# Performance work log

Hardware: AMD Instinct MI355X
Metric: run time of the kernel (lower is better)

The kernel has to match this reference:

```python
import jax, jax.numpy as jnp
import numpy as np

B, N, D, M, H = 16, 196, 512, 20, 8


def setup_inputs() -> dict:
    key = jax.random.key(0)
    ks = jax.random.split(key, 8)
    s = 0.02  # small init scale for stable activations
    return {
        "F_clean": jax.random.normal(ks[0], (B, N, D), dtype=jnp.float32),
        "in_proj_w": jax.random.normal(ks[1], (3 * D, D), dtype=jnp.float32) * s,
        "in_proj_b": jnp.zeros((3 * D,), jnp.float32),
        "out_w": jax.random.normal(ks[2], (D, D), dtype=jnp.float32) * s,
        "out_b": jnp.zeros((D,), jnp.float32),
        "w1": jax.random.normal(ks[3], (D, D), dtype=jnp.float32) * s,
        "b1": jnp.zeros((D,), jnp.float32),
        "ln_g": jnp.ones((D,), jnp.float32),
        "ln_b": jnp.zeros((D,), jnp.float32),
        "w2": jax.random.normal(ks[4], (M, D), dtype=jnp.float32) * s,
        "b2": jnp.zeros((M,), jnp.float32),
        "templates": jax.random.normal(ks[5], (M, D), dtype=jnp.float32),
        "k": 51,  # int(D * sparsity_ratio=0.1)
    }


def reference(F_clean, in_proj_w, in_proj_b, out_w, out_b, w1, b1, ln_g, ln_b, w2, b2, templates, k):
    b, n, d = F_clean.shape
    hd = d // H
    # --- MultiheadAttention (batch_first, dropout inactive at eval) ---
    qkv = F_clean @ in_proj_w.T + in_proj_b  # [B,N,3D]
    q, kk, v = jnp.split(qkv, 3, axis=-1)
    to_heads = lambda x: x.reshape(b, n, H, hd).transpose(0, 2, 1, 3)  # [B,H,N,hd]
    q, kk, v = to_heads(q), to_heads(kk), to_heads(v)
    attn = jax.nn.softmax(jnp.einsum('bhqd,bhkd->bhqk', q, kk) / jnp.sqrt(jnp.float32(hd)), axis=-1)
    o = jnp.einsum('bhqk,bhkd->bhqd', attn, v).transpose(0, 2, 1, 3).reshape(b, n, d)
    F_enh = o @ out_w.T + out_b + F_clean  # residual
    # --- decompose MLP: Linear -> LayerNorm -> GELU(exact) -> Linear ---
    h = F_enh @ w1.T + b1
    mu = h.mean(-1, keepdims=True)
    var = h.var(-1, keepdims=True)
    h = (h - mu) / jnp.sqrt(var + 1e-5) * ln_g + ln_b
    h = jax.nn.gelu(h, approximate=False)
    Qp = h @ w2.T + b2  # [B,N,M]
    # --- outer-product expansion: [B,N,D,M] ---
    Q = F_clean[:, :, :, None] * templates.T[None, None] * Qp[:, :, None, :]
    # --- per-(b,n,m) abs-topk over D, scatter 0/1 mask, L2-normalize over D ---
    A = Q.transpose(0, 1, 3, 2)  # [B,N,M,D]
    _, idx = jax.lax.top_k(jnp.abs(A), k)
    mask = jnp.put_along_axis(jnp.zeros(A.shape, A.dtype), idx, 1.0, axis=-1, inplace=False)
    Qs = A * mask
    nrm = jnp.sqrt(jnp.sum(Qs * Qs, axis=-1, keepdims=True))
    Qn = Qs / jnp.maximum(nrm, 1e-6)  # torch F.normalize clamps norm to eps
    return Qn.transpose(0, 1, 3, 2)  # [B,N,D,M]
```

## Files before the change

kernel.cpp:

```cpp
#include <hip/hip_runtime.h>
#include <cmath>


typedef __attribute__((ext_vector_type(8))) short bf16x8v;
typedef __attribute__((ext_vector_type(4))) float f32x4v;

__device__ __forceinline__ unsigned short f2bf_rne(float x) {
  unsigned u = __float_as_uint(x);
  u += 0x7fffu + ((u >> 16) & 1u);
  return (unsigned short)(u >> 16);
}
__device__ __forceinline__ float bf2f(unsigned short h) {
  return __uint_as_float(((unsigned)h) << 16);
}
__device__ __forceinline__ void split3_1(float x,
    unsigned short& s0, unsigned short& s1, unsigned short& s2) {
  s0 = f2bf_rne(x); float r1 = x - bf2f(s0);
  s1 = f2bf_rne(r1); float r2 = r1 - bf2f(s1);
  s2 = f2bf_rne(r2);
}

__global__ __launch_bounds__(256) void prep_kernel(
    const float* __restrict__ F, unsigned short* __restrict__ Fs,
    const float* __restrict__ Wqkv, const float* __restrict__ W1,
    unsigned short* __restrict__ Walls,
    const float* __restrict__ Wo, unsigned short* __restrict__ Wcs,
    float* __restrict__ Vt,
    const float* __restrict__ bo, const float* __restrict__ b1,
    float* __restrict__ bcomb,
    const float* __restrict__ bqkv, float* __restrict__ biasAll)
{
  int b = blockIdx.x;
  int tid = threadIdx.x;

  if (b < 1296) {
    const float* X; unsigned short* O; long long i8, pstride;
    if (b < 784)       { X = F;    O = Fs;              pstride = 1605632; i8 = (long long)b * 256 + tid; }
    else if (b < 1168) { X = Wqkv; O = Walls;           pstride = 1048576; i8 = (long long)(b - 784) * 256 + tid; }
    else               { X = W1;   O = Walls + 786432;  pstride = 1048576; i8 = (long long)(b - 1168) * 256 + tid; }
    const float4 aa = *(const float4*)(X + i8 * 8);
    const float4 bb = *(const float4*)(X + i8 * 8 + 4);
    float xs[8] = {aa.x, aa.y, aa.z, aa.w, bb.x, bb.y, bb.z, bb.w};
    bf16x8v o0, o1, o2;
#pragma unroll
    for (int e = 0; e < 8; e++) {
      unsigned short s0, s1, s2;
      split3_1(xs[e], s0, s1, s2);
      o0[e] = (short)s0; o1[e] = (short)s1; o2[e] = (short)s2;
    }
    *(bf16x8v*)(O + i8 * 8)               = o0;
    *(bf16x8v*)(O + pstride + i8 * 8)     = o1;
    *(bf16x8v*)(O + 2 * pstride + i8 * 8) = o2;
    return;
  }

  if (b < 1360) {
    __shared__ __align__(16) float As[16][68];
    __shared__ __align__(16) float Bs[16][68];
    int local = b - 1296;
    int i0 = (local >> 3) * 64, j0 = (local & 7) * 64;
    int tx = tid & 15, ty = tid >> 4;
    double acc[4][4];
#pragma unroll
    for (int i = 0; i < 4; i++)
#pragma unroll
      for (int j = 0; j < 4; j++) acc[i][j] = 0.0;
    for (int k0 = 0; k0 < 512; k0 += 16) {
#pragma unroll
      for (int rr = 0; rr < 4; rr++) {
        int r = ty + 16 * rr;
        As[tx][r] = W1[(size_t)(i0 + r) * 512 + k0 + tx];
      }
      {
        int j = tid & 63, c0 = (tid >> 6) * 4;
#pragma unroll
        for (int cc = 0; cc < 4; cc++) {
          int c = c0 + cc;
          Bs[c][j] = Wo[(size_t)(k0 + c) * 512 + j0 + j];
        }
      }
      __syncthreads();
      float cf[4][4];
#pragma unroll
      for (int i = 0; i < 4; i++)
#pragma unroll
        for (int j = 0; j < 4; j++) cf[i][j] = 0.0f;
#pragma unroll
      for (int kk = 0; kk < 16; kk++) {
        float4 a4 = *(const float4*)&As[kk][ty * 4];
        float4 b4 = *(const float4*)&Bs[kk][tx * 4];
        float av[4] = {a4.x, a4.y, a4.z, a4.w};
        float bv[4] = {b4.x, b4.y, b4.z, b4.w};
#pragma unroll
        for (int i = 0; i < 4; i++)
#pragma unroll
          for (int j = 0; j < 4; j++) cf[i][j] = fmaf(av[i], bv[j], cf[i][j]);
      }
#pragma unroll
      for (int i = 0; i < 4; i++)
#pragma unroll
        for (int j = 0; j < 4; j++) acc[i][j] += (double)cf[i][j];
      __syncthreads();
    }
#pragma unroll
    for (int i = 0; i < 4; i++) {
      int gi = i0 + ty * 4 + i;
#pragma unroll
      for (int j = 0; j < 4; j++) {
        int gj = j0 + tx * 4 + j;
        float o = (float)acc[i][j];
        unsigned short l0, l1, l2;
        split3_1(o, l0, l1, l2);
        size_t idx = (size_t)gi * 512 + gj;
        Wcs[idx] = l0; Wcs[idx + 262144] = l1; Wcs[idx + 524288] = l2;
      }
    }
    return;
  }

  if (b < 1472) {
    long long p0 = (long long)(b - 1360) * 2048 + tid * 8;
#pragma unroll
    for (int e = 0; e < 8; e++) {
      long long pf = p0 + e;
      int z = (int)(pf / 1792);
      int r = (int)(pf - (long long)z * 1792);
      int d = r / 28, kk = r - d * 28;
      Vt[(size_t)z * 14336 + (size_t)d * 224 + 196 + kk] = 0.0f;
    }
    return;
  }

  if (b == 1472) {
#pragma unroll
    for (int half = 0; half < 2; half++) {
      int n = tid + half * 256;
      const float* wr = W1 + (size_t)n * 512;
      double acc = 0.0;
      for (int k = 0; k < 512; k += 4) {
        float4 wv = *(const float4*)&wr[k];
        float4 bv = *(const float4*)&bo[k];
        acc += (double)wv.x * bv.x + (double)wv.y * bv.y +
               (double)wv.z * bv.z + (double)wv.w * bv.w;
      }
      bcomb[n] = (float)(acc + (double)b1[n]);
    }
    return;
  }

#pragma unroll
  for (int e = 0; e < 8; e++) {
    int idx = tid * 8 + e;
    biasAll[idx] = (idx < 1536) ? bqkv[idx] : 0.0f;
  }
}

#define GBK 32
#define AROWB 80
#define SPLIT_SZ (128 * AROWB)
#define BBASE (3 * SPLIT_SZ)

__global__ __launch_bounds__(256) void gemm_ps3_kernel(
    const unsigned short* __restrict__ As, const unsigned short* __restrict__ Bs,
    float* __restrict__ C, const float* __restrict__ bias,
    const float* __restrict__ res,
    int M, int N, int ldc, int ldres,
    long long aPlane, long long bPlane,
    int kLen, long long cZStride,
    float* __restrict__ VtOut)
{
  __shared__ __align__(16) unsigned char smem[2 * BBASE];

  int z = blockIdx.z;
  int kOff = z * kLen;
  C += (size_t)z * cZStride;

  int tid = threadIdx.x;
  int lane = tid & 63, w = tid >> 6;
  int wrow = w >> 1, wcol = w & 1;
  int i0 = blockIdx.x * 128, j0 = blockIdx.y * 128;

  int r = tid >> 1, hh = tid & 1;
  int arow = i0 + r; if (arow > M - 1) arow = M - 1;
  int brow = j0 + r; if (brow > N - 1) brow = N - 1;
  const unsigned short* ap = As + (size_t)arow * 512 + hh * 16 + kOff;
  const unsigned short* bp = Bs + (size_t)brow * 512 + hh * 16 + kOff;
  unsigned swoff = (unsigned)r * AROWB + (unsigned)hh * 32;

  f32x4v acc[4][4];
#pragma unroll
  for (int fi = 0; fi < 4; fi++)
#pragma unroll
    for (int fj = 0; fj < 4; fj++) acc[fi][fj] = (f32x4v){0.f, 0.f, 0.f, 0.f};

  unsigned fr_a = (unsigned)(wrow * 64 + (lane & 15)) * AROWB + (unsigned)(lane >> 4) * 16;
  unsigned fr_b = (unsigned)(wcol * 64 + (lane & 15)) * AROWB + (unsigned)(lane >> 4) * 16 + BBASE;

  for (int k0 = 0; k0 < kLen; k0 += GBK) {
    bf16x8v a0[3], a1[3], b0v[3], b1v[3];
#pragma unroll
    for (int s = 0; s < 3; s++) {
      a0[s]  = *(const bf16x8v*)(ap + s * aPlane + k0);
      a1[s]  = *(const bf16x8v*)(ap + s * aPlane + k0 + 8);
      b0v[s] = *(const bf16x8v*)(bp + s * bPlane + k0);
      b1v[s] = *(const bf16x8v*)(bp + s * bPlane + k0 + 8);
    }
    __syncthreads();
#pragma unroll
    for (int s = 0; s < 3; s++) {
      *(bf16x8v*)(smem + s * SPLIT_SZ + swoff)              = a0[s];
      *(bf16x8v*)(smem + s * SPLIT_SZ + swoff + 16)         = a1[s];
      *(bf16x8v*)(smem + BBASE + s * SPLIT_SZ + swoff)      = b0v[s];
      *(bf16x8v*)(smem + BBASE + s * SPLIT_SZ + swoff + 16) = b1v[s];
    }
    __syncthreads();

    bf16x8v af[4][3];
#pragma unroll
    for (int fi = 0; fi < 4; fi++)
#pragma unroll
      for (int s = 0; s < 3; s++)
        af[fi][s] = *(const bf16x8v*)(smem + s * SPLIT_SZ + fr_a + fi * (16 * AROWB));

#pragma unroll
    for (int fj = 0; fj < 4; fj++) {
      bf16x8v b0 = *(const bf16x8v*)(smem + 0 * SPLIT_SZ + fr_b + fj * (16 * AROWB));
      bf16x8v b1 = *(const bf16x8v*)(smem + 1 * SPLIT_SZ + fr_b + fj * (16 * AROWB));
      bf16x8v b2 = *(const bf16x8v*)(smem + 2 * SPLIT_SZ + fr_b + fj * (16 * AROWB));
#pragma unroll
      for (int fi = 0; fi < 4; fi++) {
        f32x4v c = acc[fi][fj];
        c = __builtin_amdgcn_mfma_f32_16x16x32_bf16(af[fi][2], b0, c, 0, 0, 0);
        c = __builtin_amdgcn_mfma_f32_16x16x32_bf16(af[fi][1], b1, c, 0, 0, 0);
        c = __builtin_amdgcn_mfma_f32_16x16x32_bf16(af[fi][0], b2, c, 0, 0, 0);
        c = __builtin_amdgcn_mfma_f32_16x16x32_bf16(af[fi][1], b0, c, 0, 0, 0);
        c = __builtin_amdgcn_mfma_f32_16x16x32_bf16(af[fi][0], b1, c, 0, 0, 0);
        c = __builtin_amdgcn_mfma_f32_16x16x32_bf16(af[fi][0], b0, c, 0, 0, 0);
        acc[fi][fj] = c;
      }
    }
  }

#pragma unroll
  for (int fi = 0; fi < 4; fi++) {
    int row0 = i0 + wrow * 64 + fi * 16 + (lane >> 4) * 4;
#pragma unroll
    for (int fj = 0; fj < 4; fj++) {
      int col = j0 + wcol * 64 + fj * 16 + (lane & 15);
      if (col >= N) continue;
      float badd = (bias && z == 0) ? bias[col] : 0.0f;
      f32x4v v = acc[fi][fj];
#pragma unroll
      for (int rr = 0; rr < 4; rr++) {
        int row = row0 + rr;
        if (row < M) {
          float o = v[rr] + badd;
          if (res && z == 0) o += res[(size_t)row * ldres + col];
          if (VtOut && col >= 1024 && col < 1536) {
            int d = col - 1024;
            int bb = row / 196;
            int kk = row - bb * 196;
            int zz = bb * 8 + (d >> 6);
            VtOut[(size_t)zz * 14336 + (size_t)(d & 63) * 224 + kk] = o;
          } else {
            C[(size_t)row * ldc + col] = o;
          }
        }
      }
    }
  }
}

__global__ __launch_bounds__(256) void gemm_bf16x3_kernel(
    const float* __restrict__ A, const float* __restrict__ B,
    float* __restrict__ C, const float* __restrict__ bias,
    const float* __restrict__ res,
    int M, int N, int K, int lda, int ldb, int ldc,
    int zInner, long long aOuter, long long aInner,
    long long bOuter, long long bInner,
    long long cOuter, long long cInner,
    unsigned short* __restrict__ Cl, long long clPlane)
{
  int z = blockIdx.z;
  int zo = z / zInner, zi = z % zInner;
  A += zo * aOuter + zi * aInner;
  B += zo * bOuter + zi * bInner;
  long long coff = zo * cOuter + zi * cInner;
  if (C) C += coff;
  if (Cl) Cl += coff;

  __shared__ __align__(16) unsigned char smem[2 * BBASE];

  int tid = threadIdx.x;
  int lane = tid & 63, w = tid >> 6;
  int wrow = w >> 1, wcol = w & 1;
  int i0 = blockIdx.x * 128, j0 = blockIdx.y * 128;

  int srow = tid >> 1;
  int skh  = tid & 1;
  int arow = i0 + srow; if (arow > M - 1) arow = M - 1;
  int brow = j0 + srow; if (brow > N - 1) brow = N - 1;
  const float* aptr = A + (size_t)arow * lda + skh * 16;
  const float* bptr = B + (size_t)brow * ldb + skh * 16;
  unsigned swoff = (unsigned)srow * AROWB + (unsigned)skh * 32;

  f32x4v acc[4][4];
#pragma unroll
  for (int fi = 0; fi < 4; fi++)
#pragma unroll
    for (int fj = 0; fj < 4; fj++) acc[fi][fj] = (f32x4v){0.f, 0.f, 0.f, 0.f};

  unsigned fr_a = (unsigned)(wrow * 64 + (lane & 15)) * AROWB + (unsigned)(lane >> 4) * 16;
  unsigned fr_b = (unsigned)(wcol * 64 + (lane & 15)) * AROWB + (unsigned)(lane >> 4) * 16 + BBASE;

  for (int k0 = 0; k0 < K; k0 += GBK) {
    float av[16], bv[16];
    {
      const float4 q0 = *(const float4*)(aptr + k0);
      const float4 q1 = *(const float4*)(aptr + k0 + 4);
      const float4 q2 = *(const float4*)(aptr + k0 + 8);
      const float4 q3 = *(const float4*)(aptr + k0 + 12);
      av[0]=q0.x; av[1]=q0.y; av[2]=q0.z; av[3]=q0.w;
      av[4]=q1.x; av[5]=q1.y; av[6]=q1.z; av[7]=q1.w;
      av[8]=q2.x; av[9]=q2.y; av[10]=q2.z; av[11]=q2.w;
      av[12]=q3.x; av[13]=q3.y; av[14]=q3.z; av[15]=q3.w;
      const float4 r0 = *(const float4*)(bptr + k0);
      const float4 r1 = *(const float4*)(bptr + k0 + 4);
      const float4 r2 = *(const float4*)(bptr + k0 + 8);
      const float4 r3 = *(const float4*)(bptr + k0 + 12);
      bv[0]=r0.x; bv[1]=r0.y; bv[2]=r0.z; bv[3]=r0.w;
      bv[4]=r1.x; bv[5]=r1.y; bv[6]=r1.z; bv[7]=r1.w;
      bv[8]=r2.x; bv[9]=r2.y; bv[10]=r2.z; bv[11]=r2.w;
      bv[12]=r3.x; bv[13]=r3.y; bv[14]=r3.z; bv[15]=r3.w;
    }
    unsigned short ha[3][16], hb[3][16];
#pragma unroll
    for (int e = 0; e < 16; e++) {
      split3_1(av[e], ha[0][e], ha[1][e], ha[2][e]);
      split3_1(bv[e], hb[0][e], hb[1][e], hb[2][e]);
    }
    __syncthreads();
#pragma unroll
    for (int s = 0; s < 3; s++) {
      bf16x8v v0, v1, w0, w1;
#pragma unroll
      for (int e = 0; e < 8; e++) {
        v0[e] = (short)ha[s][e]; v1[e] = (short)ha[s][8 + e];
        w0[e] = (short)hb[s][e]; w1[e] = (short)hb[s][8 + e];
      }
      *(bf16x8v*)(smem + s * SPLIT_SZ + swoff)              = v0;
      *(bf16x8v*)(smem + s * SPLIT_SZ + swoff + 16)         = v1;
      *(bf16x8v*)(smem + BBASE + s * SPLIT_SZ + swoff)      = w0;
      *(bf16x8v*)(smem + BBASE + s * SPLIT_SZ + swoff + 16) = w1;
    }
    __syncthreads();

    bf16x8v af[4][3];
#pragma unroll
    for (int fi = 0; fi < 4; fi++)
#pragma unroll
      for (int s = 0; s < 3; s++)
        af[fi][s] = *(const bf16x8v*)(smem + s * SPLIT_SZ + fr_a + fi * (16 * AROWB));

#pragma unroll
    for (int fj = 0; fj < 4; fj++) {
      bf16x8v b0 = *(const bf16x8v*)(smem + 0 * SPLIT_SZ + fr_b + fj * (16 * AROWB));
      bf16x8v b1 = *(const bf16x8v*)(smem + 1 * SPLIT_SZ + fr_b + fj * (16 * AROWB));
      bf16x8v b2 = *(const bf16x8v*)(smem + 2 * SPLIT_SZ + fr_b + fj * (16 * AROWB));
#pragma unroll
      for (int fi = 0; fi < 4; fi++) {
        f32x4v c = acc[fi][fj];
        c = __builtin_amdgcn_mfma_f32_16x16x32_bf16(af[fi][2], b0, c, 0, 0, 0);
        c = __builtin_amdgcn_mfma_f32_16x16x32_bf16(af[fi][1], b1, c, 0, 0, 0);
        c = __builtin_amdgcn_mfma_f32_16x16x32_bf16(af[fi][0], b2, c, 0, 0, 0);
        c = __builtin_amdgcn_mfma_f32_16x16x32_bf16(af[fi][1], b0, c, 0, 0, 0);
        c = __builtin_amdgcn_mfma_f32_16x16x32_bf16(af[fi][0], b1, c, 0, 0, 0);
        c = __builtin_amdgcn_mfma_f32_16x16x32_bf16(af[fi][0], b0, c, 0, 0, 0);
        acc[fi][fj] = c;
      }
    }
  }

#pragma unroll
  for (int fi = 0; fi < 4; fi++) {
    int row0 = i0 + wrow * 64 + fi * 16 + (lane >> 4) * 4;
#pragma unroll
    for (int fj = 0; fj < 4; fj++) {
      int col = j0 + wcol * 64 + fj * 16 + (lane & 15);
      if (col >= N) continue;
      float badd = bias ? bias[col] : 0.0f;
      f32x4v v = acc[fi][fj];
#pragma unroll
      for (int rr = 0; rr < 4; rr++) {
        int row = row0 + rr;
        if (row < M) {
          float o = v[rr] + badd;
          if (res) o += res[(size_t)row * ldc + col];
          size_t idx = (size_t)row * ldc + col;
          if (Cl) {
            unsigned short l0, l1, l2;
            split3_1(o, l0, l1, l2);
            Cl[idx] = l0; Cl[idx + clPlane] = l1; Cl[idx + 2 * clPlane] = l2;
          } else {
            C[idx] = o;
          }
        }
      }
    }
  }
}

__global__ __launch_bounds__(256) void softmax_kernel(float* __restrict__ S)
{
  int row = blockIdx.x * 4 + (threadIdx.x >> 6);
  int lane = threadIdx.x & 63;
  float* sr = S + (size_t)row * 196;
  double v[4];
#pragma unroll
  for (int t = 0; t < 4; t++) {
    int j = lane + 64 * t;
    v[t] = (j < 196) ? (double)sr[j] * 0.125 : -1e300;
  }
  double mx = fmax(fmax(v[0], v[1]), fmax(v[2], v[3]));
#pragma unroll
  for (int off = 1; off < 64; off <<= 1) mx = fmax(mx, __shfl_xor(mx, off));
  double e[4]; double s = 0.0;
#pragma unroll
  for (int t = 0; t < 4; t++) {
    int j = lane + 64 * t;
    e[t] = (j < 196) ? exp(v[t] - mx) : 0.0;
    s += e[t];
  }
#pragma unroll
  for (int off = 1; off < 64; off <<= 1) s += __shfl_xor(s, off);
  double inv = 1.0 / s;
#pragma unroll
  for (int t = 0; t < 4; t++) {
    int j = lane + 64 * t;
    if (j < 196) sr[j] = (float)(e[t] * inv);
  }
}

__global__ __launch_bounds__(256) void lnw2_kernel(
    const float* __restrict__ H, const float* __restrict__ g,
    const float* __restrict__ bb, const float* __restrict__ W2,
    const float* __restrict__ B2, float* __restrict__ Qp)
{
  int row = blockIdx.x;
  const float* hr = H + (size_t)row * 512;
  int tid = threadIdx.x, lane = tid & 63, wv = tid >> 6;
  __shared__ double red[8];
  __shared__ float y[512];
  double x0 = (double)hr[tid]       + (double)hr[tid + 1605632]
            + (double)hr[tid + 3211264] + (double)hr[tid + 4816896];
  double x1 = (double)hr[tid + 256] + (double)hr[tid + 256 + 1605632]
            + (double)hr[tid + 256 + 3211264] + (double)hr[tid + 256 + 4816896];
  double s = x0 + x1;
#pragma unroll
  for (int off = 1; off < 64; off <<= 1) s += __shfl_xor(s, off);
  if (lane == 0) red[wv] = s;
  __syncthreads();
  double mu = (red[0] + red[1] + red[2] + red[3]) * (1.0 / 512.0);
  double d0 = x0 - mu, d1 = x1 - mu;
  double q = d0 * d0 + d1 * d1;
#pragma unroll
  for (int off = 1; off < 64; off <<= 1) q += __shfl_xor(q, off);
  if (lane == 0) red[4 + wv] = q;
  __syncthreads();
  double var = (red[4] + red[5] + red[6] + red[7]) * (1.0 / 512.0);
  double inv = 1.0 / sqrt(var + 1e-5);
  double y0 = d0 * inv * (double)g[tid]       + (double)bb[tid];
  double y1 = d1 * inv * (double)g[tid + 256] + (double)bb[tid + 256];
  const double ISQRT2 = 0.70710678118654752440;
  double z0 = 0.5 * y0 * (1.0 + erf(y0 * ISQRT2));
  double z1 = 0.5 * y1 * (1.0 + erf(y1 * ISQRT2));
  y[tid] = (float)z0;
  y[tid + 256] = (float)z1;
  __syncthreads();

#pragma unroll 1
  for (int t = 0; t < 5; t++) {
    int m = wv * 5 + t;
    const float* wr = W2 + (size_t)m * 512;
    double acc = 0.0;
#pragma unroll
    for (int sE = 0; sE < 8; sE++) {
      int j = lane + 64 * sE;
      acc += (double)y[j] * (double)wr[j];
    }
#pragma unroll
    for (int off = 1; off < 64; off <<= 1) acc += __shfl_xor(acc, off);
    if (lane == 0) Qp[(size_t)row * 20 + m] = (float)(acc + (double)B2[m]);
  }
}

__device__ __forceinline__ void topk_finish32(
    const unsigned* uh, const unsigned* ul, const float* apf,
    unsigned thrh, bool exact, float qp, int g,
    unsigned long long* __restrict__ masks, float* __restrict__ qif, int lane)
{
  const int KSEL = 51;
  bool sel[8];
  if (exact) {
#pragma unroll
    for (int s = 0; s < 8; s++) sel[s] = (uh[s] >= thrh);
  } else {
    int cg = 0;
#pragma unroll
    for (int s = 0; s < 8; s++) {
      sel[s] = (uh[s] > thrh);
      cg += (int)__popcll(__ballot(sel[s]));
    }
    int need = KSEL - cg;
    bool tk[8];
#pragma unroll
    for (int s = 0; s < 8; s++) tk[s] = false;
    while (need > 0) {
      unsigned long long bk = 0ULL;
#pragma unroll
      for (int s = 0; s < 8; s++) {
        if (uh[s] == thrh && !tk[s]) {
          unsigned long long key = (1ULL << 41)
                                 | ((unsigned long long)ul[s] << 9)
                                 | ((unsigned long long)(7 - s) << 6)
                                 | (unsigned long long)(63 - lane);
          bk = key > bk ? key : bk;
        }
      }
#pragma unroll
      for (int off = 1; off < 64; off <<= 1) {
        unsigned long long ob = __shfl_xor(bk, off);
        bk = ob > bk ? ob : bk;
      }
      if ((int)(63 - (bk & 63ULL)) == lane) {
        int wsI = 7 - (int)((bk >> 6) & 7ULL);
        sel[wsI] = true;
        tk[wsI] = true;
      }
      need--;
    }
  }

  float ss = 0.f;
  unsigned long long selb[8];
#pragma unroll
  for (int s = 0; s < 8; s++) {
    selb[s] = __ballot((int)sel[s]);
    if (sel[s]) ss += apf[s] * apf[s];
  }
#pragma unroll
  for (int off = 1; off < 64; off <<= 1) ss += __shfl_xor(ss, off);
  float nrm = fabsf(qp) * sqrtf(ss);
  float qid = qp / fmaxf(nrm, 1e-6f);
  if (lane == 0) {
    qif[g] = qid;
#pragma unroll
    for (int s = 0; s < 8; s++) masks[(size_t)g * 8 + s] = selb[s];
  }
}

__global__ __launch_bounds__(256) void topk_select_kernel(
    const float* __restrict__ F, const float* __restrict__ T,
    const float* __restrict__ Qp, unsigned long long* __restrict__ masks,
    float* __restrict__ qif)
{
  const int KSEL = 51;
  int wid = blockIdx.x * 4 + (threadIdx.x >> 6);
  int lane = threadIdx.x & 63;
  int g0 = wid * 2;
  int bn = g0 / 20, m0 = g0 - bn * 20;
  const float* Frow = F + (size_t)bn * 512;
  const float* T0r = T + (size_t)m0 * 512;
  const float* T1r = T0r + 512;

  unsigned uh0[8], ul0[8], uh1[8], ul1[8];
  float ap0[8], ap1[8];
#pragma unroll
  for (int s = 0; s < 8; s++) {
    double fd = (double)Frow[lane + 64 * s];
    double p0 = fd * (double)T0r[lane + 64 * s];
    double p1 = fd * (double)T1r[lane + 64 * s];
    unsigned long long u0 =
        (unsigned long long)__double_as_longlong(p0) & 0x7fffffffffffffffULL;
    unsigned long long u1 =
        (unsigned long long)__double_as_longlong(p1) & 0x7fffffffffffffffULL;
    uh0[s] = (unsigned)(u0 >> 32); ul0[s] = (unsigned)u0;
    uh1[s] = (unsigned)(u1 >> 32); ul1[s] = (unsigned)u1;
    ap0[s] = (float)fabs(p0); ap1[s] = (float)fabs(p1);
  }

  unsigned mx0 = 0u, mn0 = 0xffffffffu, mx1 = 0u, mn1 = 0xffffffffu;
#pragma unroll
  for (int s = 0; s < 8; s++) {
    mx0 = uh0[s] > mx0 ? uh0[s] : mx0;  mn0 = uh0[s] < mn0 ? uh0[s] : mn0;
    mx1 = uh1[s] > mx1 ? uh1[s] : mx1;  mn1 = uh1[s] < mn1 ? uh1[s] : mn1;
  }
#pragma unroll
  for (int off = 1; off < 64; off <<= 1) {
    unsigned a = __shfl_xor(mx0, off); mx0 = a > mx0 ? a : mx0;
    unsigned b = __shfl_xor(mn0, off); mn0 = b < mn0 ? b : mn0;
    unsigned c = __shfl_xor(mx1, off); mx1 = c > mx1 ? c : mx1;
    unsigned d = __shfl_xor(mn1, off); mn1 = d < mn1 ? d : mn1;
  }

  unsigned lo0 = mn0, hi0 = mx0 + 1u, lo1 = mn1, hi1 = mx1 + 1u;
  bool ex0 = false, ex1 = false;
  bool dn0 = (hi0 - lo0 <= 1u), dn1 = (hi1 - lo1 <= 1u);
  while (!(dn0 && dn1)) {
    if (!dn0) {
      unsigned mid = lo0 + ((hi0 - lo0) >> 1);
      int c = 0;
#pragma unroll
      for (int s = 0; s < 8; s++) c += (int)__popcll(__ballot(uh0[s] >= mid));
      if (c >= KSEL) { lo0 = mid; if (c == KSEL) { ex0 = true; dn0 = true; } }
      else hi0 = mid;
      dn0 = dn0 || (hi0 - lo0 <= 1u);
    }
    if (!dn1) {
      unsigned mid = lo1 + ((hi1 - lo1) >> 1);
      int c = 0;
#pragma unroll
      for (int s = 0; s < 8; s++) c += (int)__popcll(__ballot(uh1[s] >= mid));
      if (c >= KSEL) { lo1 = mid; if (c == KSEL) { ex1 = true; dn1 = true; } }
      else hi1 = mid;
      dn1 = dn1 || (hi1 - lo1 <= 1u);
    }
  }
  topk_finish32(uh0, ul0, ap0, lo0, ex0, Qp[g0],     g0,     masks, qif, lane);
  topk_finish32(uh1, ul1, ap1, lo1, ex1, Qp[g0 + 1], g0 + 1, masks, qif, lane);
}

__global__ __launch_bounds__(256) void topk_write_kernel(
    const float* __restrict__ F, const float* __restrict__ T,
    const unsigned long long* __restrict__ masks,
    const float* __restrict__ qif, float* __restrict__ out)
{
  int bn = blockIdx.x;
  int tid = threadIdx.x;
  __shared__ unsigned long long mw[20][8];
  __shared__ float qf[20];
  __shared__ float vt[256][21];
  if (tid < 160) ((unsigned long long*)mw)[tid] = masks[(size_t)bn * 160 + tid];
  if (tid < 20) qf[tid] = qif[(size_t)bn * 20 + tid];
  const float* Frow = F + (size_t)bn * 512;
  float* orow = out + (size_t)bn * 10240;
  __syncthreads();

#pragma unroll
  for (int half = 0; half < 2; half++) {
    int d = half * 256 + tid;
    float fd = Frow[d];
    int dw = d >> 6, db = d & 63;
#pragma unroll
    for (int m = 0; m < 20; m++) {
      bool sel = (mw[m][dw] >> db) & 1ULL;
      float tv = T[(size_t)m * 512 + d];
      vt[tid][m] = sel ? fd * tv * qf[m] : 0.0f;
    }
    __syncthreads();
#pragma unroll
    for (int k = 0; k < 5; k++) {
      int flat = (k * 256 + tid) * 4;
      float v[4];
#pragma unroll
      for (int e = 0; e < 4; e++) {
        int fe = flat + e;
        int dl = fe / 20;
        int mm = fe - dl * 20;
        v[e] = vt[dl][mm];
      }
      float4 o = {v[0], v[1], v[2], v[3]};
      *(float4*)&orow[half * 5120 + flat] = o;
    }
    __syncthreads();
  }
}

extern "C" void kernel_launch(void* const* d_in, const int* in_sizes, int n_in,
                              void* d_out, int out_size, void* d_ws, size_t ws_size,
                              hipStream_t stream) {
  const float* F    = (const float*)d_in[0];
  const float* Wqkv = (const float*)d_in[1];
  const float* bqkv = (const float*)d_in[2];
  const float* Wo   = (const float*)d_in[3];
  const float* bo   = (const float*)d_in[4];
  const float* W1   = (const float*)d_in[5];
  const float* b1   = (const float*)d_in[6];
  const float* lng  = (const float*)d_in[7];
  const float* lnb  = (const float*)d_in[8];
  const float* W2   = (const float*)d_in[9];
  const float* b2   = (const float*)d_in[10];
  const float* Tm   = (const float*)d_in[11];
  float* out = (float*)d_out;

  float* ws = (float*)d_ws;
  float* qkvw   = ws;
  float* scores = ws + 6422528;
  float* Vt     = ws + 11339776;
  float* h1p    = ws + 13174784;
  float* Qp     = ws + 19597312;
  float* bcomb  = ws + 19660032;
  float* biasAll= ws + 19660544;
  unsigned long long* masks = (unsigned long long*)(ws + 19662592);
  float* qifb   = ws + 20666112;
  unsigned short* Fs    = (unsigned short*)(ws + 20728832);
  unsigned short* Walls = (unsigned short*)(ws + 23137280);
  unsigned short* Wcs   = (unsigned short*)(ws + 24710144);
  unsigned short* Omgs  = (unsigned short*)(ws + 25103360);
  dim3 blk(256);

  prep_kernel<<<dim3(1474), blk, 0, stream>>>(
      F, Fs, Wqkv, W1, Walls, Wo, Wcs, Vt, bo, b1, bcomb, bqkv, biasAll);

  gemm_ps3_kernel<<<dim3(25, 16, 1), blk, 0, stream>>>(
      Fs, Walls, qkvw, biasAll, nullptr,
      3136, 2048, 2048, 0, 1605632LL, 1048576LL, 512, 0LL, Vt);

  gemm_bf16x3_kernel<<<dim3(2, 2, 128), blk, 0, stream>>>(
      qkvw, qkvw + 512, scores, nullptr, nullptr,
      196, 196, 64, 2048, 2048, 196,
      8, 196LL * 2048, 64, 196LL * 2048, 64, 8LL * 38416, 38416,
      nullptr, 0);

  softmax_kernel<<<dim3(6272), blk, 0, stream>>>(scores);

  gemm_bf16x3_kernel<<<dim3(2, 1, 128), blk, 0, stream>>>(
      scores, Vt, nullptr, nullptr, nullptr,
      196, 64, 196, 196, 224, 512,
      8, 8LL * 38416, 38416, 8LL * 14336, 14336, 100352, 64,
      Omgs, 1605632LL);

  gemm_ps3_kernel<<<dim3(25, 4, 4), blk, 0, stream>>>(
      Omgs, Wcs, h1p, bcomb, qkvw + 1536,
      3136, 512, 512, 2048, 1605632LL, 262144LL, 128, 1605632LL, nullptr);

  lnw2_kernel<<<dim3(3136), blk, 0, stream>>>(h1p, lng, lnb, W2, b2, Qp);

  topk_select_kernel<<<dim3(7840), blk, 0, stream>>>(F, Tm, Qp, masks, qifb);

  topk_write_kernel<<<dim3(3136), blk, 0, stream>>>(F, Tm, masks, qifb, out);
}
```

Before: 316.0 us.

## Emit pre-split bf16 Q/K/V/P from epilogues and fuse topk select with write

The QKV GEMM epilogue now writes Q, K and transposed V directly as three-plane bf16 splits, and softmax writes the probabilities as bf16 splits. Both attention GEMMs can then reuse the pre-split gemm_ps3 kernel instead of the fp32 kernel that re-splits operands in every k-step. The topk select and output write kernels are merged into one 640-thread block per (b,n), so the mask and scale stay in shared memory and no longer round-trip through global memory. In exchange the epilogues write three planes per value, padding is stored explicitly, and the fused write kernel drops its shared-memory transpose staging.

```diff
diff --git a/kernel.cpp b/kernel.cpp
--- a/kernel.cpp
+++ b/kernel.cpp
@@ -20,12 +20,17 @@
   s2 = f2bf_rne(r2);
 }
 
+#define QK_PLANE   1605632LL
+#define VT_PLANE   1835008LL
+#define PS_PLANE   5619712LL
+#define OMG_PLANE  1605632LL
+
 __global__ __launch_bounds__(256) void prep_kernel(
     const float* __restrict__ F, unsigned short* __restrict__ Fs,
     const float* __restrict__ Wqkv, const float* __restrict__ W1,
     unsigned short* __restrict__ Walls,
     const float* __restrict__ Wo, unsigned short* __restrict__ Wcs,
-    float* __restrict__ Vt,
+    unsigned short* __restrict__ Vts,
     const float* __restrict__ bo, const float* __restrict__ b1,
     float* __restrict__ bcomb,
     const float* __restrict__ bqkv, float* __restrict__ biasAll)
@@ -118,20 +123,22 @@
     return;
   }
 
-  if (b < 1472) {
-    long long p0 = (long long)(b - 1360) * 2048 + tid * 8;
-#pragma unroll
-    for (int e = 0; e < 8; e++) {
-      long long pf = p0 + e;
-      int z = (int)(pf / 1792);
-      int r = (int)(pf - (long long)z * 1792);
-      int d = r / 28, kk = r - d * 28;
-      Vt[(size_t)z * 14336 + (size_t)d * 224 + 196 + kk] = 0.0f;
+  if (b < 1528) {
+    long long p0 = (long long)(b - 1360) * 4096 + tid * 16;
+#pragma unroll
+    for (int e = 0; e < 16; e++) {
+      long long f = p0 + e;
+      int plane = (int)(f / 229376);
+      int rem = (int)(f - (long long)plane * 229376);
+      int z = rem / 1792;
+      int r2 = rem - z * 1792;
+      int d = r2 / 28, kk = r2 - d * 28;
+      Vts[(size_t)plane * VT_PLANE + (size_t)z * 14336 + (size_t)d * 224 + 196 + kk] = 0;
     }
     return;
   }
 
-  if (b == 1472) {
+  if (b == 1528) {
 #pragma unroll
     for (int half = 0; half < 2; half++) {
       int n = tid + half * 256;
@@ -162,18 +169,26 @@
 
 __global__ __launch_bounds__(256) void gemm_ps3_kernel(
     const unsigned short* __restrict__ As, const unsigned short* __restrict__ Bs,
-    float* __restrict__ C, const float* __restrict__ bias,
-    const float* __restrict__ res,
-    int M, int N, int ldc, int ldres,
+    int M, int N, int kLen, int lda, int ldb,
     long long aPlane, long long bPlane,
-    int kLen, long long cZStride,
-    float* __restrict__ VtOut)
+    int zInner, long long aOuter, long long aInner,
+    long long bOuter, long long bInner,
+    long long cOuter, long long cInner, int kOffPerZ,
+    const float* __restrict__ bias, const float* __restrict__ res, int ldres,
+    int mode,
+    float* __restrict__ C, int ldc,
+    unsigned short* __restrict__ Cl, long long clPlane,
+    unsigned short* __restrict__ Qs, unsigned short* __restrict__ Ks,
+    unsigned short* __restrict__ Vts)
 {
   __shared__ __align__(16) unsigned char smem[2 * BBASE];
 
   int z = blockIdx.z;
-  int kOff = z * kLen;
-  C += (size_t)z * cZStride;
+  int zo = z / zInner, zi = z % zInner;
+  As += zo * aOuter + zi * aInner;
+  Bs += zo * bOuter + zi * bInner;
+  long long coff = zo * cOuter + zi * cInner;
+  int kOff = zi * kOffPerZ;
 
   int tid = threadIdx.x;
   int lane = tid & 63, w = tid >> 6;
@@ -183,8 +198,8 @@
   int r = tid >> 1, hh = tid & 1;
   int arow = i0 + r; if (arow > M - 1) arow = M - 1;
   int brow = j0 + r; if (brow > N - 1) brow = N - 1;
-  const unsigned short* ap = As + (size_t)arow * 512 + hh * 16 + kOff;
-  const unsigned short* bp = Bs + (size_t)brow * 512 + hh * 16 + kOff;
+  const unsigned short* ap = As + (size_t)arow * lda + hh * 16 + kOff;
+  const unsigned short* bp = Bs + (size_t)brow * ldb + hh * 16 + kOff;
   unsigned swoff = (unsigned)r * AROWB + (unsigned)hh * 32;
 
   f32x4v acc[4][4];
@@ -253,17 +268,35 @@
 #pragma unroll
       for (int rr = 0; rr < 4; rr++) {
         int row = row0 + rr;
-        if (row < M) {
-          float o = v[rr] + badd;
-          if (res && z == 0) o += res[(size_t)row * ldres + col];
-          if (VtOut && col >= 1024 && col < 1536) {
-            int d = col - 1024;
-            int bb = row / 196;
-            int kk = row - bb * 196;
-            int zz = bb * 8 + (d >> 6);
-            VtOut[(size_t)zz * 14336 + (size_t)(d & 63) * 224 + kk] = o;
+        if (row >= M) continue;
+        float o = v[rr] + badd;
+        if (res && z == 0) o += res[(size_t)row * ldres + col];
+        if (mode == 0) {
+          C[coff + (size_t)row * ldc + col] = o;
+        } else if (mode == 1) {
+          unsigned short l0, l1, l2;
+          split3_1(o, l0, l1, l2);
+          size_t idx = coff + (size_t)row * ldc + col;
+          Cl[idx] = l0; Cl[idx + clPlane] = l1; Cl[idx + 2 * clPlane] = l2;
+        } else {
+          int bb = row / 196, q = row - bb * 196;
+          if (col < 1024) {
+            int cc = col & 511;
+            int hd = cc >> 6, d = cc & 63;
+            unsigned short* P = (col < 512) ? Qs : Ks;
+            size_t idx = ((size_t)(bb * 8 + hd)) * 12544 + (size_t)q * 64 + d;
+            unsigned short l0, l1, l2;
+            split3_1(o, l0, l1, l2);
+            P[idx] = l0; P[idx + QK_PLANE] = l1; P[idx + 2 * QK_PLANE] = l2;
+          } else if (col < 1536) {
+            int d2 = col - 1024;
+            size_t idx = ((size_t)(bb * 8 + (d2 >> 6))) * 14336
+                       + (size_t)(d2 & 63) * 224 + q;
+            unsigned short l0, l1, l2;
+            split3_1(o, l0, l1, l2);
+            Vts[idx] = l0; Vts[idx + VT_PLANE] = l1; Vts[idx + 2 * VT_PLANE] = l2;
           } else {
-            C[(size_t)row * ldc + col] = o;
+            C[(size_t)row * 512 + (col - 1536)] = o;
           }
         }
       }
@@ -271,150 +304,12 @@
   }
 }
 
-__global__ __launch_bounds__(256) void gemm_bf16x3_kernel(
-    const float* __restrict__ A, const float* __restrict__ B,
-    float* __restrict__ C, const float* __restrict__ bias,
-    const float* __restrict__ res,
-    int M, int N, int K, int lda, int ldb, int ldc,
-    int zInner, long long aOuter, long long aInner,
-    long long bOuter, long long bInner,
-    long long cOuter, long long cInner,
-    unsigned short* __restrict__ Cl, long long clPlane)
-{
-  int z = blockIdx.z;
-  int zo = z / zInner, zi = z % zInner;
-  A += zo * aOuter + zi * aInner;
-  B += zo * bOuter + zi * bInner;
-  long long coff = zo * cOuter + zi * cInner;
-  if (C) C += coff;
-  if (Cl) Cl += coff;
-
-  __shared__ __align__(16) unsigned char smem[2 * BBASE];
-
-  int tid = threadIdx.x;
-  int lane = tid & 63, w = tid >> 6;
-  int wrow = w >> 1, wcol = w & 1;
-  int i0 = blockIdx.x * 128, j0 = blockIdx.y * 128;
-
-  int srow = tid >> 1;
-  int skh  = tid & 1;
-  int arow = i0 + srow; if (arow > M - 1) arow = M - 1;
-  int brow = j0 + srow; if (brow > N - 1) brow = N - 1;
-  const float* aptr = A + (size_t)arow * lda + skh * 16;
-  const float* bptr = B + (size_t)brow * ldb + skh * 16;
-  unsigned swoff = (unsigned)srow * AROWB + (unsigned)skh * 32;
-
-  f32x4v acc[4][4];
-#pragma unroll
-  for (int fi = 0; fi < 4; fi++)
-#pragma unroll
-    for (int fj = 0; fj < 4; fj++) acc[fi][fj] = (f32x4v){0.f, 0.f, 0.f, 0.f};
-
-  unsigned fr_a = (unsigned)(wrow * 64 + (lane & 15)) * AROWB + (unsigned)(lane >> 4) * 16;
-  unsigned fr_b = (unsigned)(wcol * 64 + (lane & 15)) * AROWB + (unsigned)(lane >> 4) * 16 + BBASE;
-
-  for (int k0 = 0; k0 < K; k0 += GBK) {
-    float av[16], bv[16];
-    {
-      const float4 q0 = *(const float4*)(aptr + k0);
-      const float4 q1 = *(const float4*)(aptr + k0 + 4);
-      const float4 q2 = *(const float4*)(aptr + k0 + 8);
-      const float4 q3 = *(const float4*)(aptr + k0 + 12);
-      av[0]=q0.x; av[1]=q0.y; av[2]=q0.z; av[3]=q0.w;
-      av[4]=q1.x; av[5]=q1.y; av[6]=q1.z; av[7]=q1.w;
-      av[8]=q2.x; av[9]=q2.y; av[10]=q2.z; av[11]=q2.w;
-      av[12]=q3.x; av[13]=q3.y; av[14]=q3.z; av[15]=q3.w;
-      const float4 r0 = *(const float4*)(bptr + k0);
-      const float4 r1 = *(const float4*)(bptr + k0 + 4);
-      const float4 r2 = *(const float4*)(bptr + k0 + 8);
-      const float4 r3 = *(const float4*)(bptr + k0 + 12);
-      bv[0]=r0.x; bv[1]=r0.y; bv[2]=r0.z; bv[3]=r0.w;
-      bv[4]=r1.x; bv[5]=r1.y; bv[6]=r1.z; bv[7]=r1.w;
-      bv[8]=r2.x; bv[9]=r2.y; bv[10]=r2.z; bv[11]=r2.w;
-      bv[12]=r3.x; bv[13]=r3.y; bv[14]=r3.z; bv[15]=r3.w;
-    }
-    unsigned short ha[3][16], hb[3][16];
-#pragma unroll
-    for (int e = 0; e < 16; e++) {
-      split3_1(av[e], ha[0][e], ha[1][e], ha[2][e]);
-      split3_1(bv[e], hb[0][e], hb[1][e], hb[2][e]);
-    }
-    __syncthreads();
-#pragma unroll
-    for (int s = 0; s < 3; s++) {
-      bf16x8v v0, v1, w0, w1;
-#pragma unroll
-      for (int e = 0; e < 8; e++) {
-        v0[e] = (short)ha[s][e]; v1[e] = (short)ha[s][8 + e];
-        w0[e] = (short)hb[s][e]; w1[e] = (short)hb[s][8 + e];
-      }
-      *(bf16x8v*)(smem + s * SPLIT_SZ + swoff)              = v0;
-      *(bf16x8v*)(smem + s * SPLIT_SZ + swoff + 16)         = v1;
-      *(bf16x8v*)(smem + BBASE + s * SPLIT_SZ + swoff)      = w0;
-      *(bf16x8v*)(smem + BBASE + s * SPLIT_SZ + swoff + 16) = w1;
-    }
-    __syncthreads();
-
-    bf16x8v af[4][3];
-#pragma unroll
-    for (int fi = 0; fi < 4; fi++)
-#pragma unroll
-      for (int s = 0; s < 3; s++)
-        af[fi][s] = *(const bf16x8v*)(smem + s * SPLIT_SZ + fr_a + fi * (16 * AROWB));
-
-#pragma unroll
-    for (int fj = 0; fj < 4; fj++) {
-      bf16x8v b0 = *(const bf16x8v*)(smem + 0 * SPLIT_SZ + fr_b + fj * (16 * AROWB));
-      bf16x8v b1 = *(const bf16x8v*)(smem + 1 * SPLIT_SZ + fr_b + fj * (16 * AROWB));
-      bf16x8v b2 = *(const bf16x8v*)(smem + 2 * SPLIT_SZ + fr_b + fj * (16 * AROWB));
-#pragma unroll
-      for (int fi = 0; fi < 4; fi++) {
-        f32x4v c = acc[fi][fj];
-        c = __builtin_amdgcn_mfma_f32_16x16x32_bf16(af[fi][2], b0, c, 0, 0, 0);
-        c = __builtin_amdgcn_mfma_f32_16x16x32_bf16(af[fi][1], b1, c, 0, 0, 0);
-        c = __builtin_amdgcn_mfma_f32_16x16x32_bf16(af[fi][0], b2, c, 0, 0, 0);
-        c = __builtin_amdgcn_mfma_f32_16x16x32_bf16(af[fi][1], b0, c, 0, 0, 0);
-        c = __builtin_amdgcn_mfma_f32_16x16x32_bf16(af[fi][0], b1, c, 0, 0, 0);
-        c = __builtin_amdgcn_mfma_f32_16x16x32_bf16(af[fi][0], b0, c, 0, 0, 0);
-        acc[fi][fj] = c;
-      }
-    }
-  }
-
-#pragma unroll
-  for (int fi = 0; fi < 4; fi++) {
-    int row0 = i0 + wrow * 64 + fi * 16 + (lane >> 4) * 4;
-#pragma unroll
-    for (int fj = 0; fj < 4; fj++) {
-      int col = j0 + wcol * 64 + fj * 16 + (lane & 15);
-      if (col >= N) continue;
-      float badd = bias ? bias[col] : 0.0f;
-      f32x4v v = acc[fi][fj];
-#pragma unroll
-      for (int rr = 0; rr < 4; rr++) {
-        int row = row0 + rr;
-        if (row < M) {
-          float o = v[rr] + badd;
-          if (res) o += res[(size_t)row * ldc + col];
-          size_t idx = (size_t)row * ldc + col;
-          if (Cl) {
-            unsigned short l0, l1, l2;
-            split3_1(o, l0, l1, l2);
-            Cl[idx] = l0; Cl[idx + clPlane] = l1; Cl[idx + 2 * clPlane] = l2;
-          } else {
-            C[idx] = o;
-          }
-        }
-      }
-    }
-  }
-}
-
-__global__ __launch_bounds__(256) void softmax_kernel(float* __restrict__ S)
+__global__ __launch_bounds__(256) void softmax_kernel(
+    const float* __restrict__ S, unsigned short* __restrict__ Ps)
 {
   int row = blockIdx.x * 4 + (threadIdx.x >> 6);
   int lane = threadIdx.x & 63;
-  float* sr = S + (size_t)row * 196;
+  const float* sr = S + (size_t)row * 196;
   double v[4];
 #pragma unroll
   for (int t = 0; t < 4; t++) {
@@ -434,10 +329,16 @@
 #pragma unroll
   for (int off = 1; off < 64; off <<= 1) s += __shfl_xor(s, off);
   double inv = 1.0 / s;
+  unsigned short* pr = Ps + (size_t)row * 224;
 #pragma unroll
   for (int t = 0; t < 4; t++) {
     int j = lane + 64 * t;
-    if (j < 196) sr[j] = (float)(e[t] * inv);
+    if (j < 224) {
+      float pv = (j < 196) ? (float)(e[t] * inv) : 0.0f;
+      unsigned short l0, l1, l2;
+      split3_1(pv, l0, l1, l2);
+      pr[j] = l0; pr[j + PS_PLANE] = l1; pr[j + 2 * PS_PLANE] = l2;
+    }
   }
 }
 
@@ -496,8 +397,8 @@
 
 __device__ __forceinline__ void topk_finish32(
     const unsigned* uh, const unsigned* ul, const float* apf,
-    unsigned thrh, bool exact, float qp, int g,
-    unsigned long long* __restrict__ masks, float* __restrict__ qif, int lane)
+    unsigned thrh, bool exact, float qp, int m,
+    unsigned long long (*mw)[8], float* qf, int lane)
 {
   const int KSEL = 51;
   bool sel[8];
@@ -553,126 +454,104 @@
   float nrm = fabsf(qp) * sqrtf(ss);
   float qid = qp / fmaxf(nrm, 1e-6f);
   if (lane == 0) {
-    qif[g] = qid;
-#pragma unroll
-    for (int s = 0; s < 8; s++) masks[(size_t)g * 8 + s] = selb[s];
-  }
-}
-
-__global__ __launch_bounds__(256) void topk_select_kernel(
+    qf[m] = qid;
+#pragma unroll
+    for (int s = 0; s < 8; s++) mw[m][s] = selb[s];
+  }
+}
+
+__global__ __launch_bounds__(640) void selwrite_kernel(
     const float* __restrict__ F, const float* __restrict__ T,
-    const float* __restrict__ Qp, unsigned long long* __restrict__ masks,
-    float* __restrict__ qif)
+    const float* __restrict__ Qp, float* __restrict__ out)
 {
   const int KSEL = 51;
-  int wid = blockIdx.x * 4 + (threadIdx.x >> 6);
-  int lane = threadIdx.x & 63;
-  int g0 = wid * 2;
-  int bn = g0 / 20, m0 = g0 - bn * 20;
-  const float* Frow = F + (size_t)bn * 512;
-  const float* T0r = T + (size_t)m0 * 512;
-  const float* T1r = T0r + 512;
-
-  unsigned uh0[8], ul0[8], uh1[8], ul1[8];
-  float ap0[8], ap1[8];
-#pragma unroll
-  for (int s = 0; s < 8; s++) {
-    double fd = (double)Frow[lane + 64 * s];
-    double p0 = fd * (double)T0r[lane + 64 * s];
-    double p1 = fd * (double)T1r[lane + 64 * s];
-    unsigned long long u0 =
-        (unsigned long long)__double_as_longlong(p0) & 0x7fffffffffffffffULL;
-    unsigned long long u1 =
-        (unsigned long long)__double_as_longlong(p1) & 0x7fffffffffffffffULL;
-    uh0[s] = (unsigned)(u0 >> 32); ul0[s] = (unsigned)u0;
-    uh1[s] = (unsigned)(u1 >> 32); ul1[s] = (unsigned)u1;
-    ap0[s] = (float)fabs(p0); ap1[s] = (float)fabs(p1);
-  }
-
-  unsigned mx0 = 0u, mn0 = 0xffffffffu, mx1 = 0u, mn1 = 0xffffffffu;
-#pragma unroll
-  for (int s = 0; s < 8; s++) {
-    mx0 = uh0[s] > mx0 ? uh0[s] : mx0;  mn0 = uh0[s] < mn0 ? uh0[s] : mn0;
-    mx1 = uh1[s] > mx1 ? uh1[s] : mx1;  mn1 = uh1[s] < mn1 ? uh1[s] : mn1;
-  }
-#pragma unroll
-  for (int off = 1; off < 64; off <<= 1) {
-    unsigned a = __shfl_xor(mx0, off); mx0 = a > mx0 ? a : mx0;
-    unsigned b = __shfl_xor(mn0, off); mn0 = b < mn0 ? b : mn0;
-    unsigned c = __shfl_xor(mx1, off); mx1 = c > mx1 ? c : mx1;
-    unsigned d = __shfl_xor(mn1, off); mn1 = d < mn1 ? d : mn1;
-  }
-
-  unsigned lo0 = mn0, hi0 = mx0 + 1u, lo1 = mn1, hi1 = mx1 + 1u;
-  bool ex0 = false, ex1 = false;
-  bool dn0 = (hi0 - lo0 <= 1u), dn1 = (hi1 - lo1 <= 1u);
-  while (!(dn0 && dn1)) {
-    if (!dn0) {
-      unsigned mid = lo0 + ((hi0 - lo0) >> 1);
-      int c = 0;
-#pragma unroll
-      for (int s = 0; s < 8; s++) c += (int)__popcll(__ballot(uh0[s] >= mid));
-      if (c >= KSEL) { lo0 = mid; if (c == KSEL) { ex0 = true; dn0 = true; } }
-      else hi0 = mid;
-      dn0 = dn0 || (hi0 - lo0 <= 1u);
-    }
-    if (!dn1) {
-      unsigned mid = lo1 + ((hi1 - lo1) >> 1);
-      int c = 0;
-#pragma unroll
-      for (int s = 0; s < 8; s++) c += (int)__popcll(__ballot(uh1[s] >= mid));
-      if (c >= KSEL) { lo1 = mid; if (c == KSEL) { ex1 = true; dn1 = true; } }
-      else hi1 = mid;
-      dn1 = dn1 || (hi1 - lo1 <= 1u);
-    }
-  }
-  topk_finish32(uh0, ul0, ap0, lo0, ex0, Qp[g0],     g0,     masks, qif, lane);
-  topk_finish32(uh1, ul1, ap1, lo1, ex1, Qp[g0 + 1], g0 + 1, masks, qif, lane);
-}
-
-__global__ __launch_bounds__(256) void topk_write_kernel(
-    const float* __restrict__ F, const float* __restrict__ T,
-    const unsigned long long* __restrict__ masks,
-    const float* __restrict__ qif, float* __restrict__ out)
-{
   int bn = blockIdx.x;
   int tid = threadIdx.x;
+  int lane = tid & 63, w = tid >> 6;
   __shared__ unsigned long long mw[20][8];
   __shared__ float qf[20];
-  __shared__ float vt[256][21];
-  if (tid < 160) ((unsigned long long*)mw)[tid] = masks[(size_t)bn * 160 + tid];
-  if (tid < 20) qf[tid] = qif[(size_t)bn * 20 + tid];
+
   const float* Frow = F + (size_t)bn * 512;
+
+  {
+    int m0 = 2 * w;
+    const float* T0r = T + (size_t)m0 * 512;
+    const float* T1r = T0r + 512;
+    unsigned uh0[8], ul0[8], uh1[8], ul1[8];
+    float ap0[8], ap1[8];
+#pragma unroll
+    for (int s = 0; s < 8; s++) {
+      double fd = (double)Frow[lane + 64 * s];
+      double p0 = fd * (double)T0r[lane + 64 * s];
+      double p1 = fd * (double)T1r[lane + 64 * s];
+      unsigned long long u0 =
+          (unsigned long long)__double_as_longlong(p0) & 0x7fffffffffffffffULL;
+      unsigned long long u1 =
+          (unsigned long long)__double_as_longlong(p1) & 0x7fffffffffffffffULL;
+      uh0[s] = (unsigned)(u0 >> 32); ul0[s] = (unsigned)u0;
+      uh1[s] = (unsigned)(u1 >> 32); ul1[s] = (unsigned)u1;
+      ap0[s] = (float)fabs(p0); ap1[s] = (float)fabs(p1);
+    }
+
+    unsigned mx0 = 0u, mn0 = 0xffffffffu, mx1 = 0u, mn1 = 0xffffffffu;
+#pragma unroll
+    for (int s = 0; s < 8; s++) {
+      mx0 = uh0[s] > mx0 ? uh0[s] : mx0;  mn0 = uh0[s] < mn0 ? uh0[s] : mn0;
+      mx1 = uh1[s] > mx1 ? uh1[s] : mx1;  mn1 = uh1[s] < mn1 ? uh1[s] : mn1;
+    }
+#pragma unroll
+    for (int off = 1; off < 64; off <<= 1) {
+      unsigned a = __shfl_xor(mx0, off); mx0 = a > mx0 ? a : mx0;
+      unsigned b = __shfl_xor(mn0, off); mn0 = b < mn0 ? b : mn0;
+      unsigned c = __shfl_xor(mx1, off); mx1 = c > mx1 ? c : mx1;
+      unsigned d = __shfl_xor(mn1, off); mn1 = d < mn1 ? d : mn1;
+    }
+
+    unsigned lo0 = mn0, hi0 = mx0 + 1u, lo1 = mn1, hi1 = mx1 + 1u;
+    bool ex0 = false, ex1 = false;
+    bool dn0 = (hi0 - lo0 <= 1u), dn1 = (hi1 - lo1 <= 1u);
+    while (!(dn0 && dn1)) {
+      if (!dn0) {
+        unsigned mid = lo0 + ((hi0 - lo0) >> 1);
+        int c = 0;
+#pragma unroll
+        for (int s = 0; s < 8; s++) c += (int)__popcll(__ballot(uh0[s] >= mid));
+        if (c >= KSEL) { lo0 = mid; if (c == KSEL) { ex0 = true; dn0 = true; } }
+        else hi0 = mid;
+        dn0 = dn0 || (hi0 - lo0 <= 1u);
+      }
+      if (!dn1) {
+        unsigned mid = lo1 + ((hi1 - lo1) >> 1);
+        int c = 0;
+#pragma unroll
+        for (int s = 0; s < 8; s++) c += (int)__popcll(__ballot(uh1[s] >= mid));
+        if (c >= KSEL) { lo1 = mid; if (c == KSEL) { ex1 = true; dn1 = true; } }
+        else hi1 = mid;
+        dn1 = dn1 || (hi1 - lo1 <= 1u);
+      }
+    }
+    int g0 = bn * 20 + m0;
+    topk_finish32(uh0, ul0, ap0, lo0, ex0, Qp[g0],     m0,     mw, qf, lane);
+    topk_finish32(uh1, ul1, ap1, lo1, ex1, Qp[g0 + 1], m0 + 1, mw, qf, lane);
+  }
+  __syncthreads();
+
   float* orow = out + (size_t)bn * 10240;
-  __syncthreads();
-
-#pragma unroll
-  for (int half = 0; half < 2; half++) {
-    int d = half * 256 + tid;
-    float fd = Frow[d];
-    int dw = d >> 6, db = d & 63;
-#pragma unroll
-    for (int m = 0; m < 20; m++) {
-      bool sel = (mw[m][dw] >> db) & 1ULL;
-      float tv = T[(size_t)m * 512 + d];
-      vt[tid][m] = sel ? fd * tv * qf[m] : 0.0f;
-    }
-    __syncthreads();
-#pragma unroll
-    for (int k = 0; k < 5; k++) {
-      int flat = (k * 256 + tid) * 4;
-      float v[4];
-#pragma unroll
-      for (int e = 0; e < 4; e++) {
-        int fe = flat + e;
-        int dl = fe / 20;
-        int mm = fe - dl * 20;
-        v[e] = vt[dl][mm];
-      }
-      float4 o = {v[0], v[1], v[2], v[3]};
-      *(float4*)&orow[half * 5120 + flat] = o;
-    }
-    __syncthreads();
+#pragma unroll
+  for (int ph = 0; ph < 4; ph++) {
+    int i = ph * 640 + tid;
+    int fe = i * 4;
+    float v[4];
+#pragma unroll
+    for (int e = 0; e < 4; e++) {
+      int f = fe + e;
+      int dd = f / 20;
+      int mm = f - dd * 20;
+      bool sel = (mw[mm][dd >> 6] >> (dd & 63)) & 1ULL;
+      v[e] = sel ? Frow[dd] * T[(size_t)mm * 512 + dd] * qf[mm] : 0.0f;
+    }
+    float4 o = {v[0], v[1], v[2], v[3]};
+    *(float4*)&orow[fe] = o;
   }
 }
 
@@ -694,49 +573,52 @@
   float* out = (float*)d_out;
 
   float* ws = (float*)d_ws;
-  float* qkvw   = ws;
-  float* scores = ws + 6422528;
-  float* Vt     = ws + 11339776;
-  float* h1p    = ws + 13174784;
-  float* Qp     = ws + 19597312;
-  float* bcomb  = ws + 19660032;
-  float* biasAll= ws + 19660544;
-  unsigned long long* masks = (unsigned long long*)(ws + 19662592);
-  float* qifb   = ws + 20666112;
-  unsigned short* Fs    = (unsigned short*)(ws + 20728832);
-  unsigned short* Walls = (unsigned short*)(ws + 23137280);
-  unsigned short* Wcs   = (unsigned short*)(ws + 24710144);
-  unsigned short* Omgs  = (unsigned short*)(ws + 25103360);
+  float* scores = ws;
+  unsigned short* Vts  = (unsigned short*)(ws + 4917248);
+  float* FW1    = ws + 7669760;
+  unsigned short* Omgs = (unsigned short*)(ws + 9275392);
+  float* h1p    = ws + 11683840;
+  float* Qp     = ws + 18106368;
+  float* bcomb  = ws + 18169088;
+  float* biasAll= ws + 18169600;
+  unsigned short* Wcs  = (unsigned short*)(ws + 18171648);
+  unsigned short* Fs   = (unsigned short*)(ws + 18564864);
+  unsigned short* Walls= (unsigned short*)(ws + 20973312);
+  unsigned short* Qs   = (unsigned short*)(ws + 22546176);
+  unsigned short* Ks   = (unsigned short*)(ws + 24954624);
+  unsigned short* Ps   = (unsigned short*)(ws + 18564864);
   dim3 blk(256);
 
-  prep_kernel<<<dim3(1474), blk, 0, stream>>>(
-      F, Fs, Wqkv, W1, Walls, Wo, Wcs, Vt, bo, b1, bcomb, bqkv, biasAll);
+  prep_kernel<<<dim3(1530), blk, 0, stream>>>(
+      F, Fs, Wqkv, W1, Walls, Wo, Wcs, Vts, bo, b1, bcomb, bqkv, biasAll);
 
   gemm_ps3_kernel<<<dim3(25, 16, 1), blk, 0, stream>>>(
-      Fs, Walls, qkvw, biasAll, nullptr,
-      3136, 2048, 2048, 0, 1605632LL, 1048576LL, 512, 0LL, Vt);
-
-  gemm_bf16x3_kernel<<<dim3(2, 2, 128), blk, 0, stream>>>(
-      qkvw, qkvw + 512, scores, nullptr, nullptr,
-      196, 196, 64, 2048, 2048, 196,
-      8, 196LL * 2048, 64, 196LL * 2048, 64, 8LL * 38416, 38416,
-      nullptr, 0);
-
-  softmax_kernel<<<dim3(6272), blk, 0, stream>>>(scores);
-
-  gemm_bf16x3_kernel<<<dim3(2, 1, 128), blk, 0, stream>>>(
-      scores, Vt, nullptr, nullptr, nullptr,
-      196, 64, 196, 196, 224, 512,
-      8, 8LL * 38416, 38416, 8LL * 14336, 14336, 100352, 64,
-      Omgs, 1605632LL);
+      Fs, Walls, 3136, 2048, 512, 512, 512, QK_PLANE, 1048576LL,
+      1, 0, 0, 0, 0, 0, 0, 0,
+      biasAll, nullptr, 0,
+      2, FW1, 512, nullptr, 0, Qs, Ks, Vts);
+
+  gemm_ps3_kernel<<<dim3(2, 2, 128), blk, 0, stream>>>(
+      Qs, Ks, 196, 196, 64, 64, 64, QK_PLANE, QK_PLANE,
+      128, 0, 12544, 0, 12544, 0, 38416, 0,
+      nullptr, nullptr, 0,
+      0, scores, 196, nullptr, 0, nullptr, nullptr, nullptr);
+
+  softmax_kernel<<<dim3(6272), blk, 0, stream>>>(scores, Ps);
+
+  gemm_ps3_kernel<<<dim3(2, 1, 128), blk, 0, stream>>>(
+      Ps, Vts, 196, 64, 224, 224, 224, PS_PLANE, VT_PLANE,
+      8, 351232, 43904, 114688, 14336, 100352, 64, 0,
+      nullptr, nullptr, 0,
+      1, nullptr, 512, Omgs, OMG_PLANE, nullptr, nullptr, nullptr);
 
   gemm_ps3_kernel<<<dim3(25, 4, 4), blk, 0, stream>>>(
-      Omgs, Wcs, h1p, bcomb, qkvw + 1536,
-      3136, 512, 512, 2048, 1605632LL, 262144LL, 128, 1605632LL, nullptr);
+      Omgs, Wcs, 3136, 512, 128, 512, 512, OMG_PLANE, 262144LL,
+      4, 0, 0, 0, 0, 0, 1605632, 128,
+      bcomb, FW1, 512,
+      0, h1p, 512, nullptr, 0, nullptr, nullptr, nullptr);
 
   lnw2_kernel<<<dim3(3136), blk, 0, stream>>>(h1p, lng, lnb, W2, b2, Qp);
 
-  topk_select_kernel<<<dim3(7840), blk, 0, stream>>>(F, Tm, Qp, masks, qifb);
-
-  topk_write_kernel<<<dim3(3136), blk, 0, stream>>>(F, Tm, masks, qifb, out);
-}
+  selwrite_kernel<<<dim3(3136), dim3(640), 0, stream>>>(F, Tm, Qp, out);
+}
```

Result: slower. 398.7 us (+26.2%).
